# Kernel optimization log

Hardware: AMD Instinct MI355X
Metric: run time of the kernel (lower is better)

## Reference

```python
import jax, jax.numpy as jnp
import numpy as np

HEADS = 16  # init_kwargs['heads']


def setup_inputs() -> dict:
    key = jax.random.key(0)
    k1, k2, k3, k4, k5, k6 = jax.random.split(key, 6)
    N, L, E = 2, 2048, 1024
    return {
        "values": jax.random.normal(k1, (N, L, E), dtype=jnp.float32),
        "key": jax.random.normal(k2, (N, L, E), dtype=jnp.float32),
        "query": jax.random.normal(k3, (N, L, E), dtype=jnp.float32),
        "mask": jax.random.randint(k4, (N, 1, L, L), 0, 2, dtype=jnp.int32),
        # fc_out: Linear(heads*head_dim=E, E) with bias
        "W_out": jax.random.normal(k5, (E, E), dtype=jnp.float32) / np.sqrt(E),
        "b_out": jax.random.normal(k6, (E,), dtype=jnp.float32) * 0.01,
    }


def reference(values, key, query, mask, W_out, b_out):
    N, Lq, E = query.shape
    Lk = key.shape[1]
    H = HEADS
    D = E // H  # head_dim = 64
    q = query.reshape(N, Lq, H, D)
    k = key.reshape(N, Lk, H, D)
    v = values.reshape(N, Lk, H, D)
    # energy: (N, H, Q, K)
    energy = jnp.einsum("nqhd,nkhd->nhqk", q, k)
    # masked_fill BEFORE scaling, as in the original
    energy = jnp.where(mask == 0, jnp.float32(-1e20), energy)
    attn = jax.nn.softmax(energy / np.float32(np.sqrt(D)), axis=3)
    out = jnp.einsum("nhqk,nkhd->nqhd", attn, v).reshape(N, Lq, H * D)
    return out @ W_out.T + b_out
```

## Files before the change

kernel.cpp:

```cpp
#include <hip/hip_runtime.h>

#define L_SEQ  2048
#define EMB    1024
#define NHEAD  16
#define HDIM   64
#define NBATCH 2
#define NT     (L_SEQ / 64)

typedef unsigned short u16;
typedef unsigned int   u32;
typedef unsigned long long u64;
typedef short bf16x8 __attribute__((ext_vector_type(8)));
typedef float f32x4  __attribute__((ext_vector_type(4)));
typedef int   i32x4  __attribute__((ext_vector_type(4)));

static __device__ __forceinline__ u16 f2bf(float x) {
    union { float f; unsigned u; } a; a.f = x;
    unsigned r = a.u + 0x7FFFu + ((a.u >> 16) & 1u);
    return (u16)(r >> 16);
}
static __device__ __forceinline__ void cvt8(const float4& a, const float4& b, u16* o, float s) {
    o[0]=f2bf(a.x*s); o[1]=f2bf(a.y*s); o[2]=f2bf(a.z*s); o[3]=f2bf(a.w*s);
    o[4]=f2bf(b.x*s); o[5]=f2bf(b.y*s); o[6]=f2bf(b.z*s); o[7]=f2bf(b.w*s);
}

static __device__ __forceinline__ u32 cvt_pk_bf16(float lo, float hi) {
    u32 r;
    asm("v_cvt_pk_bf16_f32 %0, %1, %2" : "=v"(r) : "v"(lo), "v"(hi));
    return r;
}
static __device__ __forceinline__ void permswap32(u32 &x, u32 &y) {
    asm("v_permlane32_swap_b32 %0, %1" : "+v"(x), "+v"(y));
}
static __device__ __forceinline__ void permswap16(u32 &x, u32 &y) {
    asm("v_permlane16_swap_b32 %0, %1" : "+v"(x), "+v"(y));
}

static __device__ __forceinline__ void lds_barrier() {
    asm volatile("s_waitcnt lgkmcnt(0)" ::: "memory");
    __builtin_amdgcn_s_barrier();
    __builtin_amdgcn_sched_barrier(0);
}

__global__ __launch_bounds__(256)
void prep_fused(const float* __restrict__ Qg, const float* __restrict__ Kg,
                const float* __restrict__ Vg, const int* __restrict__ Mg,
                const float* __restrict__ Wg,
                u16* __restrict__ Qb, u16* __restrict__ Kb, u16* __restrict__ Vt,
                u64* __restrict__ maskp, u16* __restrict__ Wb)
{
    const int bid = blockIdx.x;
    const int tid = threadIdx.x;
    __shared__ u16 Vl2[64][72];

    if (bid < 1024) {
        const int wave = tid >> 6;
        const int lane = tid & 63;
        const int row  = bid * 4 + wave;
        const int* mp = Mg + (size_t)row * L_SEQ + lane;
        u64* op = maskp + (size_t)row * NT;
        for (int tt = 0; tt < NT; ++tt) {
            u64 b = __ballot(mp[tt * 64] != 0);
            if (lane == 0) op[tt] = b;
        }
    } else if (bid < 2048) {
        const int b  = bid - 1024;
        const int tt = b & 31, hh = (b >> 5) & 15, nn = b >> 9;
        const int row = tid >> 2;
        const int dc  = (tid & 3) * 16;

        const size_t gin = ((size_t)(nn * L_SEQ) + tt * 64 + row) * EMB + hh * HDIM + dc;

        {
            const float qs = 0.125f * 1.44269504f;
            u16 o[16];
            cvt8(*(const float4*)(Qg + gin),     *(const float4*)(Qg + gin + 4),  o,     qs);
            cvt8(*(const float4*)(Qg + gin + 8), *(const float4*)(Qg + gin + 12), o + 8, qs);
            *(uint4*)(Qb + gin)     = *(const uint4*)o;
            *(uint4*)(Qb + gin + 8) = *(const uint4*)&o[8];
        }
        {
            u16 o[16];
            cvt8(*(const float4*)(Kg + gin),     *(const float4*)(Kg + gin + 4),  o,     1.f);
            cvt8(*(const float4*)(Kg + gin + 8), *(const float4*)(Kg + gin + 12), o + 8, 1.f);
            size_t ko = ((size_t)(nn * NHEAD + hh) * L_SEQ + tt * 64 + row) * HDIM + dc;
            *(uint4*)(Kb + ko)     = *(const uint4*)o;
            *(uint4*)(Kb + ko + 8) = *(const uint4*)&o[8];
        }
        {
            u16 o[16];
            cvt8(*(const float4*)(Vg + gin),     *(const float4*)(Vg + gin + 4),  o,     1.f);
            cvt8(*(const float4*)(Vg + gin + 8), *(const float4*)(Vg + gin + 12), o + 8, 1.f);
            #pragma unroll
            for (int j = 0; j < 16; ++j) Vl2[dc + j][row] = o[j];
        }
        __syncthreads();
        {
            const int d  = tid >> 2;
            const int kc = (tid & 3) * 16;
            size_t vo = ((size_t)(nn * NHEAD + hh) * HDIM + d) * L_SEQ + tt * 64 + kc;
            *(uint4*)(Vt + vo)     = *(const uint4*)&Vl2[d][kc];
            *(uint4*)(Vt + vo + 8) = *(const uint4*)&Vl2[d][kc + 8];
        }
    } else {
        int i = ((bid - 2048) * 256 + tid) * 8;
        float4 a = *(const float4*)(Wg + i);
        float4 b4 = *(const float4*)(Wg + i + 4);
        u16 o[8];
        cvt8(a, b4, o, 1.f);
        *(uint4*)(Wb + i) = *(const uint4*)o;
    }
}

static __device__ __forceinline__ void pv_step(
    const u32 (&Dwp)[2][8], const u16 (&Vb)[64][72],
    f32x4 (&acc)[2][4], int l16, int quad)
{
    __builtin_amdgcn_s_setprio(1);
    #pragma unroll
    for (int kc = 0; kc < 2; ++kc) {
        bf16x8 pf[2];
        #pragma unroll
        for (int qs = 0; qs < 2; ++qs) {
            u32 b0 = Dwp[qs][4 * kc + 0], b2 = Dwp[qs][4 * kc + 2];
            permswap32(b0, b2); permswap16(b0, b2);
            u32 b1 = Dwp[qs][4 * kc + 1], b3 = Dwp[qs][4 * kc + 3];
            permswap32(b1, b3); permswap16(b1, b3);
            union { i32x4 i; bf16x8 v; } pu;
            pu.i[0] = (int)b0; pu.i[1] = (int)b1; pu.i[2] = (int)b2; pu.i[3] = (int)b3;
            pf[qs] = pu.v;
        }
        #pragma unroll
        for (int dc = 0; dc < 4; ++dc) {
            bf16x8 vf = *(const bf16x8*)&Vb[dc * 16 + l16][kc * 32 + quad * 8];
            acc[0][dc] = __builtin_amdgcn_mfma_f32_16x16x32_bf16(vf, pf[0], acc[0][dc], 0, 0, 0);
            acc[1][dc] = __builtin_amdgcn_mfma_f32_16x16x32_bf16(vf, pf[1], acc[1][dc], 0, 0, 0);
        }
    }
    __builtin_amdgcn_s_setprio(0);
}

static __device__ __forceinline__ void attn_tile(
    int t, int kbuf, int vprev, int kw, int vw,
    u32 (&Dwc)[2][8], u32 (&Dwp)[2][8],
    u16 (&Kl)[2][64][72], u16 (&Vl)[4][64][72],
    const bf16x8 (&qf)[2][2], f32x4 (&acc)[2][4], float (&ls)[2][4],
    uint4& kr0, uint4& kr1, uint4& vr0, uint4& vr1,
    u64& mr0, u64& mr1,
    const u16* kbase, const u16* vbase, const u64* mbase, int mqs,
    int srow, int scol, int l16, int quad)
{
    if (t < NT - 1) {
        *(uint4*)&Kl[kw][srow][scol]     = kr0;
        *(uint4*)&Kl[kw][srow][scol + 8] = kr1;
        *(uint4*)&Vl[vw][srow][scol]     = vr0;
        *(uint4*)&Vl[vw][srow][scol + 8] = vr1;
    }
    u64 mcur0 = mr0, mcur1 = mr1;
    if (t < NT - 1) { mr0 = mbase[t + 1]; mr1 = mbase[mqs + t + 1]; }
    if (t < NT - 2) {
        const u16* kp = kbase + (size_t)((t + 2) * 64 + srow) * HDIM + scol;
        const u16* vp = vbase + (size_t)srow * L_SEQ + (t + 2) * 64 + scol;
        kr0 = *(const uint4*)kp;  kr1 = *(const uint4*)(kp + 8);
        vr0 = *(const uint4*)vp;  vr1 = *(const uint4*)(vp + 8);
    }

    const int sh = quad * 4;
    u32 mlo0 = (u32)mcur0 >> sh, mhi0 = (u32)(mcur0 >> 32) >> sh;
    u32 mlo1 = (u32)mcur1 >> sh, mhi1 = (u32)(mcur1 >> 32) >> sh;
    #pragma unroll
    for (int cc = 0; cc < 4; ++cc) {
        bf16x8 k0 = *(const bf16x8*)&Kl[kbuf][cc * 16 + l16][quad * 8];
        bf16x8 k1 = *(const bf16x8*)&Kl[kbuf][cc * 16 + l16][32 + quad * 8];
        f32x4 z0; z0[0]=0.f; z0[1]=0.f; z0[2]=0.f; z0[3]=0.f;
        f32x4 z1 = z0;
        z0 = __builtin_amdgcn_mfma_f32_16x16x32_bf16(k0, qf[0][0], z0, 0, 0, 0);
        z0 = __builtin_amdgcn_mfma_f32_16x16x32_bf16(k1, qf[0][1], z0, 0, 0, 0);
        z1 = __builtin_amdgcn_mfma_f32_16x16x32_bf16(k0, qf[1][0], z1, 0, 0, 0);
        z1 = __builtin_amdgcn_mfma_f32_16x16x32_bf16(k1, qf[1][1], z1, 0, 0, 0);

        #pragma unroll
        for (int qs = 0; qs < 2; ++qs) {
            const f32x4& z = (qs == 0) ? z0 : z1;
            u32 w = (cc < 2) ? ((qs == 0) ? mlo0 : mlo1)
                             : ((qs == 0) ? mhi0 : mhi1);
            float pv[4];
            #pragma unroll
            for (int r = 0; r < 4; ++r) {
                const int pos = (cc & 1) * 16 + r;
                int sm = (int)(w << (31 - pos)) >> 31;
                float p = __builtin_amdgcn_exp2f(z[r]);
                p = __int_as_float(__float_as_int(p) & sm);
                ls[qs][r] += p;
                pv[r] = p;
            }
            Dwc[qs][2 * cc]     = cvt_pk_bf16(pv[0], pv[1]);
            Dwc[qs][2 * cc + 1] = cvt_pk_bf16(pv[2], pv[3]);
        }
    }

    pv_step(Dwp, Vl[vprev], acc, l16, quad);

    lds_barrier();
}

__global__ __launch_bounds__(256, 2)
void attn_kernel(const u16* __restrict__ Qb, const u16* __restrict__ Kb,
                 const u16* __restrict__ Vt, const u64* __restrict__ maskp,
                 u16* __restrict__ Og)
{
    const int i    = blockIdx.x;
    const int x    = i & 7;
    const int s    = i >> 3;
    const int g    = ((s >> 4) << 3) + x;
    const int qblk = s & 15;
    const int h    = g & 15;
    const int n    = g >> 4;

    const int tid  = threadIdx.x;
    const int wave = tid >> 6;
    const int lane = tid & 63;
    const int l16  = lane & 15;
    const int quad = lane >> 4;

    __shared__ u16 Kl[2][64][72];
    __shared__ u16 Vl[4][64][72];

    const int q0 = qblk * 128 + wave * 32;

    bf16x8 qf[2][2];
    #pragma unroll
    for (int qs = 0; qs < 2; ++qs) {
        const u16* qp = Qb + ((size_t)(n * L_SEQ) + q0 + qs * 16 + l16) * EMB + h * HDIM;
        qf[qs][0] = *(const bf16x8*)(qp + quad * 8);
        qf[qs][1] = *(const bf16x8*)(qp + 32 + quad * 8);
    }

    f32x4 acc[2][4];
    #pragma unroll
    for (int qs = 0; qs < 2; ++qs)
        #pragma unroll
        for (int c = 0; c < 4; ++c)
            #pragma unroll
            for (int r = 0; r < 4; ++r) acc[qs][c][r] = 0.f;
    float ls[2][4];
    #pragma unroll
    for (int qs = 0; qs < 2; ++qs)
        #pragma unroll
        for (int r = 0; r < 4; ++r) ls[qs][r] = 0.f;

    u32 DwA[2][8], DwB[2][8];
    #pragma unroll
    for (int qs = 0; qs < 2; ++qs)
        #pragma unroll
        for (int ii = 0; ii < 8; ++ii) { DwA[qs][ii] = 0u; DwB[qs][ii] = 0u; }

    const u16* kbase = Kb + (size_t)(n * NHEAD + h) * L_SEQ * HDIM;
    const u16* vbase = Vt + (size_t)(n * NHEAD + h) * HDIM * L_SEQ;
    const u64* mbase = maskp + ((size_t)(n * L_SEQ) + q0 + l16) * NT;
    const int  mqs   = 16 * NT;

    const int srow = tid >> 2;
    const int scol = (tid & 3) * 16;

    uint4 kr0, kr1, vr0, vr1;
    u64 mr0, mr1;

    {
        const u16* kp = kbase + (size_t)srow * HDIM + scol;
        const u16* vp = vbase + (size_t)srow * L_SEQ + scol;
        kr0 = *(const uint4*)kp;  kr1 = *(const uint4*)(kp + 8);
        vr0 = *(const uint4*)vp;  vr1 = *(const uint4*)(vp + 8);
    }
    *(uint4*)&Kl[0][srow][scol]     = kr0;
    *(uint4*)&Kl[0][srow][scol + 8] = kr1;
    *(uint4*)&Vl[0][srow][scol]     = vr0;
    *(uint4*)&Vl[0][srow][scol + 8] = vr1;
    {
        u32* vz = (u32*)&Vl[3][0][0];
        #pragma unroll
        for (int ii = 0; ii < 9; ++ii) vz[tid + ii * 256] = 0u;
    }
    {
        const u16* kp = kbase + (size_t)(64 + srow) * HDIM + scol;
        const u16* vp = vbase + (size_t)srow * L_SEQ + 64 + scol;
        kr0 = *(const uint4*)kp;  kr1 = *(const uint4*)(kp + 8);
        vr0 = *(const uint4*)vp;  vr1 = *(const uint4*)(vp + 8);
    }
    mr0 = mbase[0];
    mr1 = mbase[mqs];
    __syncthreads();

    for (int j = 0; j < 8; ++j) {
        const int t = j * 4;
        attn_tile(t + 0, 0, 3, 1, 1, DwA, DwB, Kl, Vl, qf, acc, ls,
                  kr0, kr1, vr0, vr1, mr0, mr1, kbase, vbase, mbase, mqs,
                  srow, scol, l16, quad);
        attn_tile(t + 1, 1, 0, 0, 2, DwB, DwA, Kl, Vl, qf, acc, ls,
                  kr0, kr1, vr0, vr1, mr0, mr1, kbase, vbase, mbase, mqs,
                  srow, scol, l16, quad);
        attn_tile(t + 2, 0, 1, 1, 3, DwA, DwB, Kl, Vl, qf, acc, ls,
                  kr0, kr1, vr0, vr1, mr0, mr1, kbase, vbase, mbase, mqs,
                  srow, scol, l16, quad);
        attn_tile(t + 3, 1, 2, 0, 0, DwB, DwA, Kl, Vl, qf, acc, ls,
                  kr0, kr1, vr0, vr1, mr0, mr1, kbase, vbase, mbase, mqs,
                  srow, scol, l16, quad);
    }

    pv_step(DwB, Vl[3], acc, l16, quad);

    #pragma unroll
    for (int qs = 0; qs < 2; ++qs) {
        float sm = (ls[qs][0] + ls[qs][1]) + (ls[qs][2] + ls[qs][3]);
        sm += __shfl_xor(sm, 16);
        sm += __shfl_xor(sm, 32);
        float inv = 1.f / sm;

        u16* op = Og + ((size_t)(n * L_SEQ) + q0 + qs * 16 + l16) * EMB + h * HDIM + quad * 4;
        #pragma unroll
        for (int dc = 0; dc < 4; ++dc) {
            u32 u0 = cvt_pk_bf16(acc[qs][dc][0] * inv, acc[qs][dc][1] * inv);
            u32 u1 = cvt_pk_bf16(acc[qs][dc][2] * inv, acc[qs][dc][3] * inv);
            uint2 st; st.x = u0; st.y = u1;
            *(uint2*)(op + dc * 16) = st;
        }
    }
}

__global__ __launch_bounds__(256, 4)
void out_gemm(const u16* __restrict__ A, const u16* __restrict__ B,
              const float* __restrict__ bias, float* __restrict__ out)
{
    const int i  = blockIdx.x;
    const int x  = i & 7;
    const int s  = i >> 3;
    const int bm = ((s >> 4) << 3) + x;
    const int bn = s & 15;

    const int tid = threadIdx.x;
    const int wave = tid >> 6;
    const int lane = tid & 63;
    const int l16  = lane & 15;
    const int quad = lane >> 4;
    const int wr = wave >> 1, wc = wave & 1;

    __shared__ u16 Al[64][72];
    __shared__ u16 Bl[64][72];

    f32x4 acc[2][2];
    #pragma unroll
    for (int ii = 0; ii < 2; ++ii)
        #pragma unroll
        for (int j = 0; j < 2; ++j)
            #pragma unroll
            for (int r = 0; r < 4; ++r) acc[ii][j][r] = 0.f;

    const int srow = tid >> 2;
    const int kc   = (tid & 3) * 16;

    const u16* ap = A + (size_t)(bm * 64 + srow) * EMB + kc;
    const u16* bp = B + (size_t)(bn * 64 + srow) * EMB + kc;

    uint4 ar0 = *(const uint4*)ap,        ar1 = *(const uint4*)(ap + 8);
    uint4 br0 = *(const uint4*)bp,        br1 = *(const uint4*)(bp + 8);

    for (int k0 = 0; k0 < EMB; k0 += 64) {
        lds_barrier();
        *(uint4*)&Al[srow][kc]     = ar0;
        *(uint4*)&Al[srow][kc + 8] = ar1;
        *(uint4*)&Bl[srow][kc]     = br0;
        *(uint4*)&Bl[srow][kc + 8] = br1;
        if (k0 + 64 < EMB) {
            ar0 = *(const uint4*)(ap + k0 + 64);  ar1 = *(const uint4*)(ap + k0 + 72);
            br0 = *(const uint4*)(bp + k0 + 64);  br1 = *(const uint4*)(bp + k0 + 72);
        }
        lds_barrier();

        #pragma unroll
        for (int kk = 0; kk < 2; ++kk) {
            bf16x8 af[2], bfr[2];
            #pragma unroll
            for (int ii = 0; ii < 2; ++ii)
                af[ii] = *(const bf16x8*)&Al[wr * 32 + ii * 16 + l16][kk * 32 + quad * 8];
            #pragma unroll
            for (int j = 0; j < 2; ++j)
                bfr[j] = *(const bf16x8*)&Bl[wc * 32 + j * 16 + l16][kk * 32 + quad * 8];
            #pragma unroll
            for (int ii = 0; ii < 2; ++ii)
                #pragma unroll
                for (int j = 0; j < 2; ++j)
                    acc[ii][j] = __builtin_amdgcn_mfma_f32_16x16x32_bf16(af[ii], bfr[j], acc[ii][j], 0, 0, 0);
        }
    }

    #pragma unroll
    for (int j = 0; j < 2; ++j) {
        int col = bn * 64 + wc * 32 + j * 16 + l16;
        float bv = bias[col];
        #pragma unroll
        for (int ii = 0; ii < 2; ++ii) {
            int row0 = bm * 64 + wr * 32 + ii * 16 + quad * 4;
            #pragma unroll
            for (int r = 0; r < 4; ++r)
                out[(size_t)(row0 + r) * EMB + col] = acc[ii][j][r] + bv;
        }
    }
}

extern "C" void kernel_launch(void* const* d_in, const int* in_sizes, int n_in,
                              void* d_out, int out_size, void* d_ws, size_t ws_size,
                              hipStream_t stream)
{
    const float* Vg = (const float*)d_in[0];
    const float* Kg = (const float*)d_in[1];
    const float* Qg = (const float*)d_in[2];
    const int*   Mg = (const int*)d_in[3];
    const float* Wg = (const float*)d_in[4];
    const float* Bg = (const float*)d_in[5];
    float* Og = (float*)d_out;

    const size_t QKV = (size_t)NBATCH * L_SEQ * EMB;
    char* ws = (char*)d_ws;
    u16* attn_ws = (u16*)ws;
    u16* Wb      = (u16*)(ws + QKV * 2);
    u16* Qb      = (u16*)(ws + QKV * 2 + 2 * 1024 * 1024);
    u16* Kb      = Qb + QKV;
    u16* Vt      = Kb + QKV;
    u64* maskp   = (u64*)(Vt + QKV);

    prep_fused<<<dim3(2560), 256, 0, stream>>>(Qg, Kg, Vg, Mg, Wg,
                                               Qb, Kb, Vt, maskp, Wb);

    attn_kernel<<<dim3(512), 256, 0, stream>>>(Qb, Kb, Vt, maskp, attn_ws);

    out_gemm<<<dim3(1024), 256, 0, stream>>>(attn_ws, Wb, Bg, Og);
}
```

Measured before the change: 207.0 us.

## Enlarge output GEMM tiles to 128x128 with double-buffered LDS and 512 threads

The output projection GEMM now uses 128x128 tiles with 512 threads (8 waves, 64x32 per wave) and double-buffered shared memory, which drops one barrier per k-step. The grid shrinks from 1024 to 256 blocks and the grouped block swizzle is removed. The s_setprio hints around the PV MFMA step in the attention kernel are also dropped. Larger tiles mean more reuse per loaded byte and fewer barriers, but 256 blocks may underfill the GPU's compute units and register pressure rises.

```diff
diff --git a/kernel.cpp b/kernel.cpp
--- a/kernel.cpp
+++ b/kernel.cpp
@@ -116,7 +116,6 @@
     const u32 (&Dwp)[2][8], const u16 (&Vb)[64][72],
     f32x4 (&acc)[2][4], int l16, int quad)
 {
-    __builtin_amdgcn_s_setprio(1);
     #pragma unroll
     for (int kc = 0; kc < 2; ++kc) {
         bf16x8 pf[2];
@@ -137,7 +136,6 @@
             acc[1][dc] = __builtin_amdgcn_mfma_f32_16x16x32_bf16(vf, pf[1], acc[1][dc], 0, 0, 0);
         }
     }
-    __builtin_amdgcn_s_setprio(0);
 }
 
 static __device__ __forceinline__ void attn_tile(
@@ -327,29 +325,28 @@
     }
 }
 
-__global__ __launch_bounds__(256, 4)
+__global__ __launch_bounds__(512)
 void out_gemm(const u16* __restrict__ A, const u16* __restrict__ B,
               const float* __restrict__ bias, float* __restrict__ out)
 {
     const int i  = blockIdx.x;
-    const int x  = i & 7;
-    const int s  = i >> 3;
-    const int bm = ((s >> 4) << 3) + x;
-    const int bn = s & 15;
+    const int bn = i & 7;
+    const int bm = i >> 3;
 
     const int tid = threadIdx.x;
     const int wave = tid >> 6;
     const int lane = tid & 63;
     const int l16  = lane & 15;
     const int quad = lane >> 4;
-    const int wr = wave >> 1, wc = wave & 1;
-
-    __shared__ u16 Al[64][72];
-    __shared__ u16 Bl[64][72];
-
-    f32x4 acc[2][2];
-    #pragma unroll
-    for (int ii = 0; ii < 2; ++ii)
+    const int wr = wave >> 2;
+    const int wc = wave & 3;
+
+    __shared__ u16 Al[2][128][72];
+    __shared__ u16 Bl[2][128][72];
+
+    f32x4 acc[4][2];
+    #pragma unroll
+    for (int ii = 0; ii < 4; ++ii)
         #pragma unroll
         for (int j = 0; j < 2; ++j)
             #pragma unroll
@@ -358,35 +355,37 @@
     const int srow = tid >> 2;
     const int kc   = (tid & 3) * 16;
 
-    const u16* ap = A + (size_t)(bm * 64 + srow) * EMB + kc;
-    const u16* bp = B + (size_t)(bn * 64 + srow) * EMB + kc;
+    const u16* ap = A + (size_t)(bm * 128 + srow) * EMB + kc;
+    const u16* bp = B + (size_t)(bn * 128 + srow) * EMB + kc;
 
     uint4 ar0 = *(const uint4*)ap,        ar1 = *(const uint4*)(ap + 8);
     uint4 br0 = *(const uint4*)bp,        br1 = *(const uint4*)(bp + 8);
 
-    for (int k0 = 0; k0 < EMB; k0 += 64) {
+    #pragma unroll 4
+    for (int s = 0; s < 16; ++s) {
+        const int b = s & 1;
+        *(uint4*)&Al[b][srow][kc]     = ar0;
+        *(uint4*)&Al[b][srow][kc + 8] = ar1;
+        *(uint4*)&Bl[b][srow][kc]     = br0;
+        *(uint4*)&Bl[b][srow][kc + 8] = br1;
+        if (s < 15) {
+            const int k0 = (s + 1) * 64;
+            ar0 = *(const uint4*)(ap + k0);      ar1 = *(const uint4*)(ap + k0 + 8);
+            br0 = *(const uint4*)(bp + k0);      br1 = *(const uint4*)(bp + k0 + 8);
+        }
         lds_barrier();
-        *(uint4*)&Al[srow][kc]     = ar0;
-        *(uint4*)&Al[srow][kc + 8] = ar1;
-        *(uint4*)&Bl[srow][kc]     = br0;
-        *(uint4*)&Bl[srow][kc + 8] = br1;
-        if (k0 + 64 < EMB) {
-            ar0 = *(const uint4*)(ap + k0 + 64);  ar1 = *(const uint4*)(ap + k0 + 72);
-            br0 = *(const uint4*)(bp + k0 + 64);  br1 = *(const uint4*)(bp + k0 + 72);
-        }
-        lds_barrier();
 
         #pragma unroll
         for (int kk = 0; kk < 2; ++kk) {
-            bf16x8 af[2], bfr[2];
-            #pragma unroll
-            for (int ii = 0; ii < 2; ++ii)
-                af[ii] = *(const bf16x8*)&Al[wr * 32 + ii * 16 + l16][kk * 32 + quad * 8];
+            bf16x8 af[4], bfr[2];
+            #pragma unroll
+            for (int ii = 0; ii < 4; ++ii)
+                af[ii] = *(const bf16x8*)&Al[b][wr * 64 + ii * 16 + l16][kk * 32 + quad * 8];
             #pragma unroll
             for (int j = 0; j < 2; ++j)
-                bfr[j] = *(const bf16x8*)&Bl[wc * 32 + j * 16 + l16][kk * 32 + quad * 8];
-            #pragma unroll
-            for (int ii = 0; ii < 2; ++ii)
+                bfr[j] = *(const bf16x8*)&Bl[b][wc * 32 + j * 16 + l16][kk * 32 + quad * 8];
+            #pragma unroll
+            for (int ii = 0; ii < 4; ++ii)
                 #pragma unroll
                 for (int j = 0; j < 2; ++j)
                     acc[ii][j] = __builtin_amdgcn_mfma_f32_16x16x32_bf16(af[ii], bfr[j], acc[ii][j], 0, 0, 0);
@@ -395,11 +394,11 @@
 
     #pragma unroll
     for (int j = 0; j < 2; ++j) {
-        int col = bn * 64 + wc * 32 + j * 16 + l16;
+        int col = bn * 128 + wc * 32 + j * 16 + l16;
         float bv = bias[col];
         #pragma unroll
-        for (int ii = 0; ii < 2; ++ii) {
-            int row0 = bm * 64 + wr * 32 + ii * 16 + quad * 4;
+        for (int ii = 0; ii < 4; ++ii) {
+            int row0 = bm * 128 + wr * 64 + ii * 16 + quad * 4;
             #pragma unroll
             for (int r = 0; r < 4; ++r)
                 out[(size_t)(row0 + r) * EMB + col] = acc[ii][j][r] + bv;
@@ -433,5 +432,5 @@
 
     attn_kernel<<<dim3(512), 256, 0, stream>>>(Qb, Kb, Vt, maskp, attn_ws);
 
-    out_gemm<<<dim3(1024), 256, 0, stream>>>(attn_ws, Wb, Bg, Og);
-}
+    out_gemm<<<dim3(256), 512, 0, stream>>>(attn_ws, Wb, Bg, Og);
+}
```

Result: no change. 207.8 us (+0.4%).
